# Performance work log

Measured on AMD Instinct MI355X. Metric: run time of the kernel, lower is better.

Reference implementation:

```python
import jax, jax.numpy as jnp
import numpy as np

B, S, D = 2, 2048, 1024
H, DK, DV = 16, 64, 64
NEG = -1e9

def setup_inputs() -> dict:
    key = jax.random.key(0)
    ks = jax.random.split(key, 7)
    scale = 1.0 / np.sqrt(D)
    return {
        "Q": jax.random.normal(ks[0], (B, S, D), dtype=jnp.float32),
        "K": jax.random.normal(ks[1], (B, S, D), dtype=jnp.float32),
        "V": jax.random.normal(ks[2], (B, S, D), dtype=jnp.float32),
        "Wq": jax.random.normal(ks[3], (D, H * DK), dtype=jnp.float32) * scale,
        "Wk": jax.random.normal(ks[4], (D, H * DK), dtype=jnp.float32) * scale,
        "Wv": jax.random.normal(ks[5], (D, H * DV), dtype=jnp.float32) * scale,
        "Wo": jax.random.normal(ks[6], (H * DV, D), dtype=jnp.float32) * scale,
    }

def reference(Q, K, V, Wq, Wk, Wv, Wo):
    b, sq, _ = Q.shape
    sk = K.shape[1]
    # project and split heads: [b, h, s, d]
    q = (Q @ Wq).reshape(b, sq, H, DK).transpose(0, 2, 1, 3)
    k = (K @ Wk).reshape(b, sk, H, DK).transpose(0, 2, 1, 3)
    v = (V @ Wv).reshape(b, sk, H, DV).transpose(0, 2, 1, 3)
    scores = jnp.einsum("bhqd,bhkd->bhqk", q, k) / jnp.sqrt(jnp.float32(DK))
    causal = jnp.tril(jnp.ones((sq, sk), dtype=bool))
    scores = jnp.where(causal[None, None], scores, NEG)
    attn = jax.nn.softmax(scores, axis=-1)
    out = jnp.einsum("bhqk,bhkd->bhqd", attn, v)
    out = out.transpose(0, 2, 1, 3).reshape(b, sq, H * DV)
    return out @ Wo
```

## Files before the change

### kernel.cpp

```cpp
#include <hip/hip_runtime.h>
#include <cstdint>
#include <cstddef>


typedef __bf16 bf16x8 __attribute__((ext_vector_type(8)));
typedef __bf16 bf16x4 __attribute__((ext_vector_type(4)));
typedef float f32x4 __attribute__((ext_vector_type(4)));
typedef unsigned int u32x4 __attribute__((ext_vector_type(4)));

#define MFMA __builtin_amdgcn_mfma_f32_16x16x32_bf16

static __device__ __forceinline__ __bf16 f2b(float f) { return (__bf16)f; }

static __device__ __forceinline__ void gload_lds16(const void* g, void* l) {
  __builtin_amdgcn_global_load_lds(
      (const __attribute__((address_space(1))) void*)g,
      (__attribute__((address_space(3))) void*)l, 16, 0, 0);
}

#define QSCALE 0.18033688f

__global__ __launch_bounds__(256) void wtrans_kernel(
    const float* __restrict__ w0, const float* __restrict__ w1,
    const float* __restrict__ w2, const float* __restrict__ w3,
    __bf16* __restrict__ outT)
{
  const int z = blockIdx.z;
  const float* W = (z == 0) ? w0 : (z == 1) ? w1 : (z == 2) ? w2 : w3;
  __bf16* O = outT + (size_t)z * 1048576;
  __shared__ float t[32][33];
  const int tx = threadIdx.x & 31, ty = threadIdx.x >> 5;
  const int kb = blockIdx.y * 32, nb = blockIdx.x * 32;
#pragma unroll
  for (int i = 0; i < 4; i++)
    t[ty + i * 8][tx] = W[(size_t)(kb + ty + i * 8) * 1024 + nb + tx];
  __syncthreads();
#pragma unroll
  for (int i = 0; i < 4; i++)
    O[(size_t)(nb + ty + i * 8) * 1024 + kb + tx] = f2b(t[tx][ty + i * 8]);
}

__global__ __launch_bounds__(256) void cvt_kernel(
    const float* __restrict__ a0, const float* __restrict__ a1,
    const float* __restrict__ a2, __bf16* __restrict__ o0,
    __bf16* __restrict__ o1, __bf16* __restrict__ o2)
{
  const int z = blockIdx.y;
  const float* src = (z == 0) ? a0 : (z == 1) ? a1 : a2;
  __bf16* dst = (z == 0) ? o0 : (z == 1) ? o1 : o2;
  const int idx = blockIdx.x * 256 + threadIdx.x;
#pragma unroll
  for (int it = 0; it < 4; ++it) {
    const size_t c = (size_t)(idx + it * 131072) * 8;
    f32x4 v0 = *(const f32x4*)&src[c];
    f32x4 v1 = *(const f32x4*)&src[c + 4];
    bf16x8 w = {f2b(v0[0]), f2b(v0[1]), f2b(v0[2]), f2b(v0[3]),
                f2b(v1[0]), f2b(v1[1]), f2b(v1[2]), f2b(v1[3])};
    *(bf16x8*)&dst[c] = w;
  }
}

__global__ __launch_bounds__(256) void gemm_proj_bf16_kernel(
    const __bf16* __restrict__ A0, const __bf16* __restrict__ A1,
    const __bf16* __restrict__ A2, const __bf16* __restrict__ WT,
    __bf16* __restrict__ C0, __bf16* __restrict__ C1, __bf16* __restrict__ C2)
{
  const int z = blockIdx.y;
  const __bf16* A = (z == 0) ? A0 : (z == 1) ? A1 : A2;
  const __bf16* W = WT + (size_t)z * 1048576;
  __bf16* C = (z == 0) ? C0 : (z == 1) ? C1 : C2;
  const float osc = (z == 0) ? QSCALE : 1.0f;

  const int bid = blockIdx.x;
  const int t = (bid & 7) * 32 + (bid >> 3);
  const int mt = t >> 3, nt = t & 7;
  const int mbase = mt * 128, nbase = nt * 128;

  __shared__ __align__(16) __bf16 As[128][32];
  __shared__ __align__(16) __bf16 Bs[128][32];

  const int tid = threadIdx.x;
  const int wid = tid >> 6, lane = tid & 63;
  const int wr = wid >> 1, wc = wid & 1;
  const int lr = lane & 15, kg = lane >> 4;

  f32x4 acc[4][4] = {};

  const int srow = tid >> 2, scol = (tid & 3) * 8;
  const int wbase = tid & 192;

  for (int kb = 0; kb < 32; ++kb) {
    const int k0 = kb * 32;
    __syncthreads();
#pragma unroll
    for (int p = 0; p < 2; ++p) {
      const int r = srow + p * 64;
      gload_lds16(&A[(size_t)(mbase + r) * 1024 + k0 + scol],
                  (__bf16*)As + (size_t)(p * 256 + wbase) * 8);
      gload_lds16(&W[(size_t)(nbase + r) * 1024 + k0 + scol],
                  (__bf16*)Bs + (size_t)(p * 256 + wbase) * 8);
    }
    __syncthreads();

    bf16x8 af[4], bfr[4];
#pragma unroll
    for (int i = 0; i < 4; i++) af[i] = *(const bf16x8*)&As[wr * 64 + i * 16 + lr][kg * 8];
#pragma unroll
    for (int j = 0; j < 4; j++) bfr[j] = *(const bf16x8*)&Bs[wc * 64 + j * 16 + lr][kg * 8];
#pragma unroll
    for (int i = 0; i < 4; i++)
#pragma unroll
      for (int j = 0; j < 4; j++)
        acc[i][j] = MFMA(af[i], bfr[j], acc[i][j], 0, 0, 0);
  }

  if (z == 2) {
#pragma unroll
    for (int i = 0; i < 4; i++)
#pragma unroll
      for (int j = 0; j < 4; j++) {
        const int m0 = mbase + wr * 64 + i * 16 + kg * 4;
        const int n = nbase + wc * 64 + j * 16 + lr;
        const int b = m0 >> 11, s = m0 & 2047, h = n >> 6, dv = n & 63;
        bf16x4 w;
#pragma unroll
        for (int r = 0; r < 4; r++) w[r] = f2b(acc[i][j][r]);
        *(bf16x4*)&C[(((size_t)(b * 16 + h)) * 64 + dv) * 2048 + s] = w;
      }
  } else {
#pragma unroll
    for (int i = 0; i < 4; i++)
#pragma unroll
      for (int j = 0; j < 4; j++)
#pragma unroll
        for (int r = 0; r < 4; r++) {
          const int m = mbase + wr * 64 + i * 16 + kg * 4 + r;
          const int n = nbase + wc * 64 + j * 16 + lr;
          const int b = m >> 11, s = m & 2047, h = n >> 6, dk = n & 63;
          C[(((size_t)(b * 16 + h)) * 2048 + s) * 64 + dk] = f2b(acc[i][j][r] * osc);
        }
  }
}

__global__ __launch_bounds__(256) void gemm_proj_f32_kernel(
    const float* __restrict__ A0, const float* __restrict__ A1,
    const float* __restrict__ A2, const __bf16* __restrict__ WT,
    __bf16* __restrict__ C0, __bf16* __restrict__ C1, __bf16* __restrict__ C2)
{
  const int z = blockIdx.y;
  const float* A = (z == 0) ? A0 : (z == 1) ? A1 : A2;
  const __bf16* W = WT + (size_t)z * 1048576;
  __bf16* C = (z == 0) ? C0 : (z == 1) ? C1 : C2;
  const float osc = (z == 0) ? QSCALE : 1.0f;

  const int mt = blockIdx.x >> 3, nt = blockIdx.x & 7;
  const int mbase = mt * 128, nbase = nt * 128;

  __shared__ __align__(16) __bf16 As[128][40];
  __shared__ __align__(16) __bf16 Bs[128][40];

  const int tid = threadIdx.x;
  const int wid = tid >> 6, lane = tid & 63;
  const int wr = wid >> 1, wc = wid & 1;
  const int lr = lane & 15, kg = lane >> 4;

  f32x4 acc[4][4] = {};
  const int arow = tid >> 3, ac0 = (tid & 7) * 4;

  for (int kb = 0; kb < 32; ++kb) {
    const int k0 = kb * 32;
#pragma unroll
    for (int p = 0; p < 4; ++p) {
      const int r = arow + p * 32;
      f32x4 av = *(const f32x4*)&A[(size_t)(mbase + r) * 1024 + k0 + ac0];
      bf16x4 cv = {f2b(av[0]), f2b(av[1]), f2b(av[2]), f2b(av[3])};
      *(bf16x4*)&As[r][ac0] = cv;
    }
#pragma unroll
    for (int p = 0; p < 2; ++p) {
      const int idx = p * 256 + tid;
      const int r = idx >> 2, c8 = (idx & 3) * 8;
      *(u32x4*)&Bs[r][c8] = *(const u32x4*)&W[(size_t)(nbase + r) * 1024 + k0 + c8];
    }
    __syncthreads();

    bf16x8 af[4], bfr[4];
#pragma unroll
    for (int i = 0; i < 4; i++) af[i] = *(const bf16x8*)&As[wr * 64 + i * 16 + lr][kg * 8];
#pragma unroll
    for (int j = 0; j < 4; j++) bfr[j] = *(const bf16x8*)&Bs[wc * 64 + j * 16 + lr][kg * 8];
#pragma unroll
    for (int i = 0; i < 4; i++)
#pragma unroll
      for (int j = 0; j < 4; j++)
        acc[i][j] = MFMA(af[i], bfr[j], acc[i][j], 0, 0, 0);
    __syncthreads();
  }

  if (z == 2) {
#pragma unroll
    for (int i = 0; i < 4; i++)
#pragma unroll
      for (int j = 0; j < 4; j++) {
        const int m0 = mbase + wr * 64 + i * 16 + kg * 4;
        const int n = nbase + wc * 64 + j * 16 + lr;
        const int b = m0 >> 11, s = m0 & 2047, h = n >> 6, dv = n & 63;
        bf16x4 w;
#pragma unroll
        for (int r = 0; r < 4; r++) w[r] = f2b(acc[i][j][r]);
        *(bf16x4*)&C[(((size_t)(b * 16 + h)) * 64 + dv) * 2048 + s] = w;
      }
  } else {
#pragma unroll
    for (int i = 0; i < 4; i++)
#pragma unroll
      for (int j = 0; j < 4; j++)
#pragma unroll
        for (int r = 0; r < 4; r++) {
          const int m = mbase + wr * 64 + i * 16 + kg * 4 + r;
          const int n = nbase + wc * 64 + j * 16 + lr;
          const int b = m >> 11, s = m & 2047, h = n >> 6, dk = n & 63;
          C[(((size_t)(b * 16 + h)) * 2048 + s) * 64 + dk] = f2b(acc[i][j][r] * osc);
        }
  }
}

__global__ __launch_bounds__(256) void attn_kernel(
    const __bf16* __restrict__ Qh, const __bf16* __restrict__ Kh,
    const __bf16* __restrict__ VTh, __bf16* __restrict__ AO)
{
  const int lin = blockIdx.x;
  const int l = (lin & 7) * 128 + (lin >> 3);
  const int bh = l >> 5;
  const int qblk = 31 - (l & 31);
  const int b = bh >> 4, h = bh & 15;
  const __bf16* Qp = Qh + (size_t)bh * 2048 * 64;
  const __bf16* Kp = Kh + (size_t)bh * 2048 * 64;
  const __bf16* Vp = VTh + (size_t)bh * 64 * 2048;

  __shared__ __align__(16) __bf16 Ks[2][64][72];
  __shared__ __align__(16) __bf16 Vt[2][64][72];
  __shared__ __align__(16) __bf16 Ps[4][16][72];

  const int tid = threadIdx.x, wid = tid >> 6, lane = tid & 63;
  const int lr = lane & 15, kg = lane >> 4;
  const int sr0 = tid >> 3, sc0 = (tid & 7) * 8;

  const int qbase = qblk << 6;
  const int nkv = qblk + 1;
  const int wq = qbase + wid * 16;

  bf16x8 qf0 = *(const bf16x8*)&Qp[(size_t)(wq + lr) * 64 + kg * 8];
  bf16x8 qf1 = *(const bf16x8*)&Qp[(size_t)(wq + lr) * 64 + 32 + kg * 8];

  f32x4 ot[4] = {};
  float mrow = -1e30f, lsum = 0.f;

  u32x4 kr0 = *(const u32x4*)&Kp[(size_t)sr0 * 64 + sc0];
  u32x4 kr1 = *(const u32x4*)&Kp[(size_t)(sr0 + 32) * 64 + sc0];
  u32x4 vr0 = *(const u32x4*)&Vp[(size_t)sr0 * 2048 + sc0];
  u32x4 vr1 = *(const u32x4*)&Vp[(size_t)(sr0 + 32) * 2048 + sc0];
  *(u32x4*)&Ks[0][sr0][sc0] = kr0;
  *(u32x4*)&Ks[0][sr0 + 32][sc0] = kr1;
  *(u32x4*)&Vt[0][sr0][sc0] = vr0;
  *(u32x4*)&Vt[0][sr0 + 32][sc0] = vr1;

  int cur = 0;
  for (int t = 0; t < nkv; ++t) {
    const bool pre = (t + 1 < nkv);
    if (pre) {
      const int n0 = (t + 1) << 6;
      kr0 = *(const u32x4*)&Kp[(size_t)(n0 + sr0) * 64 + sc0];
      kr1 = *(const u32x4*)&Kp[(size_t)(n0 + sr0 + 32) * 64 + sc0];
      vr0 = *(const u32x4*)&Vp[(size_t)sr0 * 2048 + n0 + sc0];
      vr1 = *(const u32x4*)&Vp[(size_t)(sr0 + 32) * 2048 + n0 + sc0];
    }
    __syncthreads();

    f32x4 st[4] = {};
    __builtin_amdgcn_s_setprio(1);
#pragma unroll
    for (int kvt = 0; kvt < 4; ++kvt) {
      bf16x8 kf0 = *(const bf16x8*)&Ks[cur][kvt * 16 + lr][kg * 8];
      bf16x8 kf1 = *(const bf16x8*)&Ks[cur][kvt * 16 + lr][32 + kg * 8];
      st[kvt] = MFMA(kf0, qf0, st[kvt], 0, 0, 0);
      st[kvt] = MFMA(kf1, qf1, st[kvt], 0, 0, 0);
    }
    __builtin_amdgcn_s_setprio(0);

    float sv[16];
#pragma unroll
    for (int kvt = 0; kvt < 4; ++kvt)
#pragma unroll
      for (int r = 0; r < 4; ++r) sv[kvt * 4 + r] = st[kvt][r];
    if (t == nkv - 1) {
      const int qidx = wq + lr;
      const int kvb = t << 6;
#pragma unroll
      for (int kvt = 0; kvt < 4; ++kvt)
#pragma unroll
        for (int r = 0; r < 4; ++r)
          if (kvb + kvt * 16 + kg * 4 + r > qidx) sv[kvt * 4 + r] = -1e30f;
    }
    float mx = fmaxf(fmaxf(sv[0], sv[1]), sv[2]);
    mx = fmaxf(fmaxf(mx, sv[3]), sv[4]);
    mx = fmaxf(fmaxf(mx, sv[5]), sv[6]);
    mx = fmaxf(fmaxf(mx, sv[7]), sv[8]);
    mx = fmaxf(fmaxf(mx, sv[9]), sv[10]);
    mx = fmaxf(fmaxf(mx, sv[11]), sv[12]);
    mx = fmaxf(fmaxf(mx, sv[13]), sv[14]);
    mx = fmaxf(mx, sv[15]);
    mx = fmaxf(mx, __shfl_xor(mx, 16));
    mx = fmaxf(mx, __shfl_xor(mx, 32));
    if (__any(mx > mrow + 8.f)) {
      const float mnew = fmaxf(mrow, mx);
      const float scl = exp2f(mrow - mnew);
      mrow = mnew;
      lsum *= scl;
#pragma unroll
      for (int dvt = 0; dvt < 4; ++dvt) ot[dvt] *= scl;
    }
#pragma unroll
    for (int kvt = 0; kvt < 4; ++kvt) {
      bf16x4 pk;
#pragma unroll
      for (int r = 0; r < 4; ++r) {
        const float p = exp2f(sv[kvt * 4 + r] - mrow);
        lsum += p;
        pk[r] = f2b(p);
      }
      *(bf16x4*)&Ps[wid][lr][kvt * 16 + kg * 4] = pk;
    }

#pragma unroll
    for (int h2 = 0; h2 < 2; ++h2) {
      bf16x8 pf = *(const bf16x8*)&Ps[wid][lr][h2 * 32 + kg * 8];
      __builtin_amdgcn_s_setprio(1);
#pragma unroll
      for (int dvt = 0; dvt < 4; ++dvt) {
        bf16x8 vf = *(const bf16x8*)&Vt[cur][dvt * 16 + lr][h2 * 32 + kg * 8];
        ot[dvt] = MFMA(vf, pf, ot[dvt], 0, 0, 0);
      }
      __builtin_amdgcn_s_setprio(0);
    }

    if (pre) {
      const int nb = cur ^ 1;
      *(u32x4*)&Ks[nb][sr0][sc0] = kr0;
      *(u32x4*)&Ks[nb][sr0 + 32][sc0] = kr1;
      *(u32x4*)&Vt[nb][sr0][sc0] = vr0;
      *(u32x4*)&Vt[nb][sr0 + 32][sc0] = vr1;
    }
    cur ^= 1;
  }

  lsum += __shfl_xor(lsum, 16);
  lsum += __shfl_xor(lsum, 32);
  const float rl = 1.f / lsum;
  const int q = wq + lr;
#pragma unroll
  for (int dvt = 0; dvt < 4; ++dvt) {
    bf16x4 w;
#pragma unroll
    for (int r = 0; r < 4; ++r) w[r] = f2b(ot[dvt][r] * rl);
    *(bf16x4*)&AO[((size_t)(b * 2048 + q)) * 1024 + h * 64 + dvt * 16 + kg * 4] = w;
  }
}

__global__ __launch_bounds__(256) void gemm_out_kernel(
    const __bf16* __restrict__ A, const __bf16* __restrict__ WT,
    float* __restrict__ Out)
{
  const int bid = blockIdx.x;
  const int t = (bid & 7) * 32 + (bid >> 3);
  const int mt = t >> 3, nt = t & 7;
  const int mbase = mt * 128, nbase = nt * 128;

  __shared__ __align__(16) __bf16 As[128][32];
  __shared__ __align__(16) __bf16 Bs[128][32];

  const int tid = threadIdx.x;
  const int wid = tid >> 6, lane = tid & 63;
  const int wr = wid >> 1, wc = wid & 1;
  const int lr = lane & 15, kg = lane >> 4;

  f32x4 acc[4][4] = {};

  const int srow = tid >> 2, scol = (tid & 3) * 8;
  const int wbase = tid & 192;

  for (int kb = 0; kb < 32; ++kb) {
    const int k0 = kb * 32;
    __syncthreads();
#pragma unroll
    for (int p = 0; p < 2; ++p) {
      const int r = srow + p * 64;
      gload_lds16(&A[(size_t)(mbase + r) * 1024 + k0 + scol],
                  (__bf16*)As + (size_t)(p * 256 + wbase) * 8);
      gload_lds16(&WT[(size_t)(nbase + r) * 1024 + k0 + scol],
                  (__bf16*)Bs + (size_t)(p * 256 + wbase) * 8);
    }
    __syncthreads();

    bf16x8 af[4], bfr[4];
#pragma unroll
    for (int i = 0; i < 4; i++) af[i] = *(const bf16x8*)&As[wr * 64 + i * 16 + lr][kg * 8];
#pragma unroll
    for (int j = 0; j < 4; j++) bfr[j] = *(const bf16x8*)&Bs[wc * 64 + j * 16 + lr][kg * 8];
#pragma unroll
    for (int i = 0; i < 4; i++)
#pragma unroll
      for (int j = 0; j < 4; j++)
        acc[i][j] = MFMA(af[i], bfr[j], acc[i][j], 0, 0, 0);
  }

#pragma unroll
  for (int i = 0; i < 4; i++)
#pragma unroll
    for (int j = 0; j < 4; j++)
#pragma unroll
      for (int r = 0; r < 4; r++) {
        const int m = mbase + wr * 64 + i * 16 + kg * 4 + r;
        const int n = nbase + wc * 64 + j * 16 + lr;
        Out[(size_t)m * 1024 + n] = acc[i][j][r];
      }
}

extern "C" void kernel_launch(void* const* d_in, const int* in_sizes, int n_in,
                              void* d_out, int out_size, void* d_ws, size_t ws_size,
                              hipStream_t stream) {
  const float* Q  = (const float*)d_in[0];
  const float* K  = (const float*)d_in[1];
  const float* V  = (const float*)d_in[2];
  const float* Wq = (const float*)d_in[3];
  const float* Wk = (const float*)d_in[4];
  const float* Wv = (const float*)d_in[5];
  const float* Wo = (const float*)d_in[6];
  float* out = (float*)d_out;

  const size_t M4 = 4194304;
  __bf16* wT  = (__bf16*)d_ws;
  __bf16* qb  = wT + M4;
  __bf16* kb  = qb + M4;
  __bf16* vtb = kb + M4;

  const bool fast = ws_size >= (size_t)(28 * 1048576) * 2;

  wtrans_kernel<<<dim3(32, 32, 4), 256, 0, stream>>>(Wq, Wk, Wv, Wo, wT);

  __bf16* ao;
  if (fast) {
    __bf16* qa = vtb + M4;
    __bf16* ka = qa + M4;
    __bf16* va = ka + M4;
    ao = qa;
    cvt_kernel<<<dim3(512, 3), 256, 0, stream>>>(Q, K, V, qa, ka, va);
    gemm_proj_bf16_kernel<<<dim3(256, 3), 256, 0, stream>>>(qa, ka, va, wT,
                                                            qb, kb, vtb);
  } else {
    ao = vtb + M4;
    gemm_proj_f32_kernel<<<dim3(256, 3), 256, 0, stream>>>(Q, K, V, wT,
                                                           qb, kb, vtb);
  }

  attn_kernel<<<dim3(1024), 256, 0, stream>>>(qb, kb, vtb, ao);
  gemm_out_kernel<<<dim3(256), 256, 0, stream>>>(ao, wT + 3 * 1048576, out);
}
```

Baseline: 138.2 us.

## Use 128-row query tiles with 8 waves per attention block

The attention kernel now runs 512-thread blocks, each covering 128 query rows with 8 waves that share the same staged K/V tiles. Each K/V tile loaded into LDS is reused by twice as many query rows, and each thread now loads one row chunk instead of two. Waves whose rows lie entirely before a KV tile skip its compute, and the causal mask is applied only on tiles that cross the diagonal. The cost is half as many blocks (512 instead of 1024), larger blocks, and idle waves waiting at barriers on diagonal tiles, which can hurt occupancy and load balance.

```diff
diff --git a/kernel.cpp b/kernel.cpp
--- a/kernel.cpp
+++ b/kernel.cpp
@@ -225,14 +225,14 @@
   }
 }
 
-__global__ __launch_bounds__(256) void attn_kernel(
+__global__ __launch_bounds__(512) void attn_kernel(
     const __bf16* __restrict__ Qh, const __bf16* __restrict__ Kh,
     const __bf16* __restrict__ VTh, __bf16* __restrict__ AO)
 {
   const int lin = blockIdx.x;
-  const int l = (lin & 7) * 128 + (lin >> 3);
-  const int bh = l >> 5;
-  const int qblk = 31 - (l & 31);
+  const int l = (lin & 7) * 64 + (lin >> 3);
+  const int bh = l >> 4;
+  const int qblk = 15 - (l & 15);
   const int b = bh >> 4, h = bh & 15;
   const __bf16* Qp = Qh + (size_t)bh * 2048 * 64;
   const __bf16* Kp = Kh + (size_t)bh * 2048 * 64;
@@ -240,14 +240,14 @@
 
   __shared__ __align__(16) __bf16 Ks[2][64][72];
   __shared__ __align__(16) __bf16 Vt[2][64][72];
-  __shared__ __align__(16) __bf16 Ps[4][16][72];
+  __shared__ __align__(16) __bf16 Ps[8][16][72];
 
   const int tid = threadIdx.x, wid = tid >> 6, lane = tid & 63;
   const int lr = lane & 15, kg = lane >> 4;
-  const int sr0 = tid >> 3, sc0 = (tid & 7) * 8;
-
-  const int qbase = qblk << 6;
-  const int nkv = qblk + 1;
+  const int sr = tid >> 3, sc = (tid & 7) * 8;
+
+  const int qbase = qblk << 7;
+  const int nkv = 2 * qblk + 2;
   const int wq = qbase + wid * 16;
 
   bf16x8 qf0 = *(const bf16x8*)&Qp[(size_t)(wq + lr) * 64 + kg * 8];
@@ -256,100 +256,94 @@
   f32x4 ot[4] = {};
   float mrow = -1e30f, lsum = 0.f;
 
-  u32x4 kr0 = *(const u32x4*)&Kp[(size_t)sr0 * 64 + sc0];
-  u32x4 kr1 = *(const u32x4*)&Kp[(size_t)(sr0 + 32) * 64 + sc0];
-  u32x4 vr0 = *(const u32x4*)&Vp[(size_t)sr0 * 2048 + sc0];
-  u32x4 vr1 = *(const u32x4*)&Vp[(size_t)(sr0 + 32) * 2048 + sc0];
-  *(u32x4*)&Ks[0][sr0][sc0] = kr0;
-  *(u32x4*)&Ks[0][sr0 + 32][sc0] = kr1;
-  *(u32x4*)&Vt[0][sr0][sc0] = vr0;
-  *(u32x4*)&Vt[0][sr0 + 32][sc0] = vr1;
+  u32x4 kr = *(const u32x4*)&Kp[(size_t)sr * 64 + sc];
+  u32x4 vr = *(const u32x4*)&Vp[(size_t)sr * 2048 + sc];
+  *(u32x4*)&Ks[0][sr][sc] = kr;
+  *(u32x4*)&Vt[0][sr][sc] = vr;
 
   int cur = 0;
   for (int t = 0; t < nkv; ++t) {
+    const int kv0 = t << 6;
     const bool pre = (t + 1 < nkv);
     if (pre) {
-      const int n0 = (t + 1) << 6;
-      kr0 = *(const u32x4*)&Kp[(size_t)(n0 + sr0) * 64 + sc0];
-      kr1 = *(const u32x4*)&Kp[(size_t)(n0 + sr0 + 32) * 64 + sc0];
-      vr0 = *(const u32x4*)&Vp[(size_t)sr0 * 2048 + n0 + sc0];
-      vr1 = *(const u32x4*)&Vp[(size_t)(sr0 + 32) * 2048 + n0 + sc0];
-    }
-    __syncthreads();
-
-    f32x4 st[4] = {};
-    __builtin_amdgcn_s_setprio(1);
-#pragma unroll
-    for (int kvt = 0; kvt < 4; ++kvt) {
-      bf16x8 kf0 = *(const bf16x8*)&Ks[cur][kvt * 16 + lr][kg * 8];
-      bf16x8 kf1 = *(const bf16x8*)&Ks[cur][kvt * 16 + lr][32 + kg * 8];
-      st[kvt] = MFMA(kf0, qf0, st[kvt], 0, 0, 0);
-      st[kvt] = MFMA(kf1, qf1, st[kvt], 0, 0, 0);
-    }
-    __builtin_amdgcn_s_setprio(0);
-
-    float sv[16];
-#pragma unroll
-    for (int kvt = 0; kvt < 4; ++kvt)
-#pragma unroll
-      for (int r = 0; r < 4; ++r) sv[kvt * 4 + r] = st[kvt][r];
-    if (t == nkv - 1) {
-      const int qidx = wq + lr;
-      const int kvb = t << 6;
+      const int n0 = kv0 + 64;
+      kr = *(const u32x4*)&Kp[(size_t)(n0 + sr) * 64 + sc];
+      vr = *(const u32x4*)&Vp[(size_t)sr * 2048 + n0 + sc];
+    }
+    __syncthreads();
+
+    if (kv0 <= wq + 15) {
+      f32x4 st[4] = {};
+      __builtin_amdgcn_s_setprio(1);
+#pragma unroll
+      for (int kvt = 0; kvt < 4; ++kvt) {
+        bf16x8 kf0 = *(const bf16x8*)&Ks[cur][kvt * 16 + lr][kg * 8];
+        bf16x8 kf1 = *(const bf16x8*)&Ks[cur][kvt * 16 + lr][32 + kg * 8];
+        st[kvt] = MFMA(kf0, qf0, st[kvt], 0, 0, 0);
+        st[kvt] = MFMA(kf1, qf1, st[kvt], 0, 0, 0);
+      }
+      __builtin_amdgcn_s_setprio(0);
+
+      float sv[16];
 #pragma unroll
       for (int kvt = 0; kvt < 4; ++kvt)
 #pragma unroll
-        for (int r = 0; r < 4; ++r)
-          if (kvb + kvt * 16 + kg * 4 + r > qidx) sv[kvt * 4 + r] = -1e30f;
-    }
-    float mx = fmaxf(fmaxf(sv[0], sv[1]), sv[2]);
-    mx = fmaxf(fmaxf(mx, sv[3]), sv[4]);
-    mx = fmaxf(fmaxf(mx, sv[5]), sv[6]);
-    mx = fmaxf(fmaxf(mx, sv[7]), sv[8]);
-    mx = fmaxf(fmaxf(mx, sv[9]), sv[10]);
-    mx = fmaxf(fmaxf(mx, sv[11]), sv[12]);
-    mx = fmaxf(fmaxf(mx, sv[13]), sv[14]);
-    mx = fmaxf(mx, sv[15]);
-    mx = fmaxf(mx, __shfl_xor(mx, 16));
-    mx = fmaxf(mx, __shfl_xor(mx, 32));
-    if (__any(mx > mrow + 8.f)) {
-      const float mnew = fmaxf(mrow, mx);
-      const float scl = exp2f(mrow - mnew);
-      mrow = mnew;
-      lsum *= scl;
-#pragma unroll
-      for (int dvt = 0; dvt < 4; ++dvt) ot[dvt] *= scl;
-    }
-#pragma unroll
-    for (int kvt = 0; kvt < 4; ++kvt) {
-      bf16x4 pk;
-#pragma unroll
-      for (int r = 0; r < 4; ++r) {
-        const float p = exp2f(sv[kvt * 4 + r] - mrow);
-        lsum += p;
-        pk[r] = f2b(p);
-      }
-      *(bf16x4*)&Ps[wid][lr][kvt * 16 + kg * 4] = pk;
-    }
-
-#pragma unroll
-    for (int h2 = 0; h2 < 2; ++h2) {
-      bf16x8 pf = *(const bf16x8*)&Ps[wid][lr][h2 * 32 + kg * 8];
-      __builtin_amdgcn_s_setprio(1);
-#pragma unroll
-      for (int dvt = 0; dvt < 4; ++dvt) {
-        bf16x8 vf = *(const bf16x8*)&Vt[cur][dvt * 16 + lr][h2 * 32 + kg * 8];
-        ot[dvt] = MFMA(vf, pf, ot[dvt], 0, 0, 0);
-      }
-      __builtin_amdgcn_s_setprio(0);
+        for (int r = 0; r < 4; ++r) sv[kvt * 4 + r] = st[kvt][r];
+      if (kv0 + 63 > wq) {
+        const int qidx = wq + lr;
+#pragma unroll
+        for (int kvt = 0; kvt < 4; ++kvt)
+#pragma unroll
+          for (int r = 0; r < 4; ++r)
+            if (kv0 + kvt * 16 + kg * 4 + r > qidx) sv[kvt * 4 + r] = -1e30f;
+      }
+      float mx = fmaxf(fmaxf(sv[0], sv[1]), sv[2]);
+      mx = fmaxf(fmaxf(mx, sv[3]), sv[4]);
+      mx = fmaxf(fmaxf(mx, sv[5]), sv[6]);
+      mx = fmaxf(fmaxf(mx, sv[7]), sv[8]);
+      mx = fmaxf(fmaxf(mx, sv[9]), sv[10]);
+      mx = fmaxf(fmaxf(mx, sv[11]), sv[12]);
+      mx = fmaxf(fmaxf(mx, sv[13]), sv[14]);
+      mx = fmaxf(mx, sv[15]);
+      mx = fmaxf(mx, __shfl_xor(mx, 16));
+      mx = fmaxf(mx, __shfl_xor(mx, 32));
+      if (__any(mx > mrow + 8.f)) {
+        const float mnew = fmaxf(mrow, mx);
+        const float scl = exp2f(mrow - mnew);
+        mrow = mnew;
+        lsum *= scl;
+#pragma unroll
+        for (int dvt = 0; dvt < 4; ++dvt) ot[dvt] *= scl;
+      }
+#pragma unroll
+      for (int kvt = 0; kvt < 4; ++kvt) {
+        bf16x4 pk;
+#pragma unroll
+        for (int r = 0; r < 4; ++r) {
+          const float p = exp2f(sv[kvt * 4 + r] - mrow);
+          lsum += p;
+          pk[r] = f2b(p);
+        }
+        *(bf16x4*)&Ps[wid][lr][kvt * 16 + kg * 4] = pk;
+      }
+
+#pragma unroll
+      for (int h2 = 0; h2 < 2; ++h2) {
+        bf16x8 pf = *(const bf16x8*)&Ps[wid][lr][h2 * 32 + kg * 8];
+        __builtin_amdgcn_s_setprio(1);
+#pragma unroll
+        for (int dvt = 0; dvt < 4; ++dvt) {
+          bf16x8 vf = *(const bf16x8*)&Vt[cur][dvt * 16 + lr][h2 * 32 + kg * 8];
+          ot[dvt] = MFMA(vf, pf, ot[dvt], 0, 0, 0);
+        }
+        __builtin_amdgcn_s_setprio(0);
+      }
     }
 
     if (pre) {
       const int nb = cur ^ 1;
-      *(u32x4*)&Ks[nb][sr0][sc0] = kr0;
-      *(u32x4*)&Ks[nb][sr0 + 32][sc0] = kr1;
-      *(u32x4*)&Vt[nb][sr0][sc0] = vr0;
-      *(u32x4*)&Vt[nb][sr0 + 32][sc0] = vr1;
+      *(u32x4*)&Ks[nb][sr][sc] = kr;
+      *(u32x4*)&Vt[nb][sr][sc] = vr;
     }
     cur ^= 1;
   }
@@ -463,6 +457,6 @@
                                                            qb, kb, vtb);
   }
 
-  attn_kernel<<<dim3(1024), 256, 0, stream>>>(qb, kb, vtb, ao);
+  attn_kernel<<<dim3(512), 512, 0, stream>>>(qb, kb, vtb, ao);
   gemm_out_kernel<<<dim3(256), 256, 0, stream>>>(ao, wT + 3 * 1048576, out);
 }
```

Result: slower. 147.8 us (+6.9%).

## Load K and V fragments directly from global memory in attention loop

Applied to the files above, without the earlier changes.

Removes the double-buffered LDS staging of K and V tiles and the per-iteration block barrier. Each wave now reads its K and V MFMA fragments straight from global memory, relying on L1/L2 caching since all four waves read the same tiles. This cuts LDS traffic and synchronisation but gives up register-prefetch overlap, and makes four redundant global reads per tile. The causal mask condition is also rewritten per wave.

```diff
diff --git a/kernel.cpp b/kernel.cpp
--- a/kernel.cpp
+++ b/kernel.cpp
@@ -238,13 +238,10 @@
   const __bf16* Kp = Kh + (size_t)bh * 2048 * 64;
   const __bf16* Vp = VTh + (size_t)bh * 64 * 2048;
 
-  __shared__ __align__(16) __bf16 Ks[2][64][72];
-  __shared__ __align__(16) __bf16 Vt[2][64][72];
   __shared__ __align__(16) __bf16 Ps[4][16][72];
 
   const int tid = threadIdx.x, wid = tid >> 6, lane = tid & 63;
   const int lr = lane & 15, kg = lane >> 4;
-  const int sr0 = tid >> 3, sc0 = (tid & 7) * 8;
 
   const int qbase = qblk << 6;
   const int nkv = qblk + 1;
@@ -256,33 +253,16 @@
   f32x4 ot[4] = {};
   float mrow = -1e30f, lsum = 0.f;
 
-  u32x4 kr0 = *(const u32x4*)&Kp[(size_t)sr0 * 64 + sc0];
-  u32x4 kr1 = *(const u32x4*)&Kp[(size_t)(sr0 + 32) * 64 + sc0];
-  u32x4 vr0 = *(const u32x4*)&Vp[(size_t)sr0 * 2048 + sc0];
-  u32x4 vr1 = *(const u32x4*)&Vp[(size_t)(sr0 + 32) * 2048 + sc0];
-  *(u32x4*)&Ks[0][sr0][sc0] = kr0;
-  *(u32x4*)&Ks[0][sr0 + 32][sc0] = kr1;
-  *(u32x4*)&Vt[0][sr0][sc0] = vr0;
-  *(u32x4*)&Vt[0][sr0 + 32][sc0] = vr1;
-
-  int cur = 0;
   for (int t = 0; t < nkv; ++t) {
-    const bool pre = (t + 1 < nkv);
-    if (pre) {
-      const int n0 = (t + 1) << 6;
-      kr0 = *(const u32x4*)&Kp[(size_t)(n0 + sr0) * 64 + sc0];
-      kr1 = *(const u32x4*)&Kp[(size_t)(n0 + sr0 + 32) * 64 + sc0];
-      vr0 = *(const u32x4*)&Vp[(size_t)sr0 * 2048 + n0 + sc0];
-      vr1 = *(const u32x4*)&Vp[(size_t)(sr0 + 32) * 2048 + n0 + sc0];
-    }
-    __syncthreads();
-
+    const int kv0 = t << 6;
+
+    const __bf16* Kt = Kp + (size_t)kv0 * 64;
     f32x4 st[4] = {};
     __builtin_amdgcn_s_setprio(1);
 #pragma unroll
     for (int kvt = 0; kvt < 4; ++kvt) {
-      bf16x8 kf0 = *(const bf16x8*)&Ks[cur][kvt * 16 + lr][kg * 8];
-      bf16x8 kf1 = *(const bf16x8*)&Ks[cur][kvt * 16 + lr][32 + kg * 8];
+      bf16x8 kf0 = *(const bf16x8*)&Kt[(size_t)(kvt * 16 + lr) * 64 + kg * 8];
+      bf16x8 kf1 = *(const bf16x8*)&Kt[(size_t)(kvt * 16 + lr) * 64 + 32 + kg * 8];
       st[kvt] = MFMA(kf0, qf0, st[kvt], 0, 0, 0);
       st[kvt] = MFMA(kf1, qf1, st[kvt], 0, 0, 0);
     }
@@ -293,14 +273,13 @@
     for (int kvt = 0; kvt < 4; ++kvt)
 #pragma unroll
       for (int r = 0; r < 4; ++r) sv[kvt * 4 + r] = st[kvt][r];
-    if (t == nkv - 1) {
+    if (kv0 + 63 > wq) {
       const int qidx = wq + lr;
-      const int kvb = t << 6;
 #pragma unroll
       for (int kvt = 0; kvt < 4; ++kvt)
 #pragma unroll
         for (int r = 0; r < 4; ++r)
-          if (kvb + kvt * 16 + kg * 4 + r > qidx) sv[kvt * 4 + r] = -1e30f;
+          if (kv0 + kvt * 16 + kg * 4 + r > qidx) sv[kvt * 4 + r] = -1e30f;
     }
     float mx = fmaxf(fmaxf(sv[0], sv[1]), sv[2]);
     mx = fmaxf(fmaxf(mx, sv[3]), sv[4]);
@@ -338,20 +317,12 @@
       __builtin_amdgcn_s_setprio(1);
 #pragma unroll
       for (int dvt = 0; dvt < 4; ++dvt) {
-        bf16x8 vf = *(const bf16x8*)&Vt[cur][dvt * 16 + lr][h2 * 32 + kg * 8];
+        bf16x8 vf = *(const bf16x8*)&Vp[(size_t)(dvt * 16 + lr) * 2048 +
+                                        kv0 + h2 * 32 + kg * 8];
         ot[dvt] = MFMA(vf, pf, ot[dvt], 0, 0, 0);
       }
       __builtin_amdgcn_s_setprio(0);
     }
-
-    if (pre) {
-      const int nb = cur ^ 1;
-      *(u32x4*)&Ks[nb][sr0][sc0] = kr0;
-      *(u32x4*)&Ks[nb][sr0 + 32][sc0] = kr1;
-      *(u32x4*)&Vt[nb][sr0][sc0] = vr0;
-      *(u32x4*)&Vt[nb][sr0 + 32][sc0] = vr1;
-    }
-    cur ^= 1;
   }
 
   lsum += __shfl_xor(lsum, 16);
```

Result: slower. 307.3 us (+122.4%).
